# Kernel optimization log

Hardware: AMD Instinct MI355X
Metric: run time of the kernel (lower is better)

The kernel has to match this reference:

```python
import jax, jax.numpy as jnp
import numpy as np

BATCH = 1024
INPUT_DIM = 256
UNITS = 256
GRID_SIZE = 5
SPLINE_ORDER = 3
GRID_LO, GRID_HI = -1.0, 1.0


def _make_grid(dtype):
    # (input_dim, grid_size + 2*spline_order + 1) uniform knot grid, extended
    # by spline_order cells on each side (matches DenseKAN.build)
    bound = GRID_HI - GRID_LO
    g = jnp.linspace(GRID_LO - SPLINE_ORDER * bound / GRID_SIZE,
                     GRID_HI + SPLINE_ORDER * bound / GRID_SIZE,
                     GRID_SIZE + 2 * SPLINE_ORDER + 1, dtype=dtype)
    return jnp.broadcast_to(g[None, :], (INPUT_DIM, g.shape[0]))


def _spline_bases(x, grid):
    # x: (B, in), grid: (in, G+2k+1) -> bases: (B, in, G+k)  (Cox-de Boor)
    xe = x[:, :, None]
    bases = ((xe >= grid[:, :-1]) & (xe < grid[:, 1:])).astype(x.dtype)
    for k in range(1, SPLINE_ORDER + 1):
        left = (xe - grid[:, :-(k + 1)]) / (grid[:, k:-1] - grid[:, :-(k + 1)])
        right = (grid[:, k + 1:] - xe) / (grid[:, k + 1:] - grid[:, 1:-k])
        bases = left * bases[:, :, :-1] + right * bases[:, :, 1:]
    return bases


def setup_inputs() -> dict:
    key = jax.random.key(0)
    k1, k2, k3 = jax.random.split(key, 3)
    x = jax.random.uniform(k1, (BATCH, INPUT_DIM), dtype=jnp.float32,
                           minval=-1.0, maxval=1.0)
    # RandomNormal(stddev=0.1) init for spline_kernel
    spline_kernel = 0.1 * jax.random.normal(
        k2, (INPUT_DIM, GRID_SIZE + SPLINE_ORDER, UNITS), dtype=jnp.float32)
    # GlorotUniform init for scale_factor
    limit = float(np.sqrt(6.0 / (INPUT_DIM + UNITS)))
    scale_factor = jax.random.uniform(k3, (INPUT_DIM, UNITS), dtype=jnp.float32,
                                      minval=-limit, maxval=limit)
    bias = jnp.zeros((UNITS,), dtype=jnp.float32)
    return {"x": x, "spline_kernel": spline_kernel,
            "scale_factor": scale_factor, "bias": bias}


def reference(x, spline_kernel, scale_factor, bias):
    grid = _make_grid(x.dtype)
    bases = _spline_bases(x, grid)                       # (B, in, G+k)
    spline_out = jnp.einsum('bik,iko->bio', bases, spline_kernel)  # (B, in, units)
    spline_out = spline_out + jax.nn.silu(x)[:, :, None]
    spline_out = spline_out * scale_factor[None, :, :]
    out = jnp.sum(spline_out, axis=-2) + bias            # (B, units)
    return out
```

## Files before the change

kernel.cpp:

```cpp
#include <hip/hip_runtime.h>
#include <hip/hip_bf16.h>

#define BATCH   1024
#define IN_DIM  256
#define UNITS   256

using short8 = __attribute__((ext_vector_type(8))) short;
using f32x4  = __attribute__((ext_vector_type(4))) float;

#define A_ELEMS (64 * 72 * 512)
#define W_ELEMS (16 * 72 * 512)

__device__ __forceinline__ unsigned short f2bf(float v) {
    __hip_bfloat16 h = __float2bfloat16(v);
    return *reinterpret_cast<unsigned short*>(&h);
}

__global__ __launch_bounds__(256) void prep_all(const float* __restrict__ X,
                                                const float* __restrict__ SK,
                                                const float* __restrict__ SF,
                                                unsigned short* __restrict__ Ap,
                                                unsigned short* __restrict__ Wp) {
    const int t = threadIdx.x;
    if (blockIdx.x < 256) {
        __shared__ unsigned short tile[18 * 512];
        const int mt = blockIdx.x >> 2;
        const int q  = blockIdx.x & 3;
        #pragma unroll
        for (int rr = 0; rr < 4; ++rr) {
            const int p  = t + 256 * rr;
            const int b  = p >> 6;
            const int il = p & 63;
            const int i  = q * 64 + il;
            const float x = X[(mt * 16 + b) * IN_DIM + i];
            const float u = (x + 2.2f) * 2.5f;
            int j = (int)floorf(u);
            j = j < 3 ? 3 : (j > 7 ? 7 : j);
            const float gj = -2.2f + 0.4f * (float)j;
            const float tt = (x - gj) * 2.5f;
            const float t2 = tt * tt, t3 = t2 * tt;
            const float k6 = 1.f / 6.f;
            const float b0 = (1.f - 3.f * tt + 3.f * t2 - t3) * k6;
            const float b1 = (3.f * t3 - 6.f * t2 + 4.f) * k6;
            const float b2 = (-3.f * t3 + 3.f * t2 + 3.f * tt + 1.f) * k6;
            const float b3 = t3 * k6;
            const float sil = x / (1.f + __expf(-x));
            const int base = j - 3;
            const int kk0  = il * 9;
            #pragma unroll
            for (int kf = 0; kf < 9; ++kf) {
                float v;
                if (kf == 8) v = sil;
                else v = (kf == base)     ? b0
                       : (kf == base + 1) ? b1
                       : (kf == base + 2) ? b2
                       : (kf == base + 3) ? b3 : 0.f;
                const int kkl  = kk0 + kf;
                const int sl   = kkl >> 5;
                const int kpos = kkl & 31;
                tile[sl * 512 + ((b | ((kpos >> 3) << 4)) << 3) + (kpos & 7)] = f2bf(v);
            }
        }
        __syncthreads();
        const unsigned int* src = (const unsigned int*)tile;
        unsigned int* dst = (unsigned int*)Ap + (mt * 72 + 18 * q) * 256;
        #pragma unroll
        for (int k = 0; k < 18; ++k) dst[t + 256 * k] = src[t + 256 * k];
    } else {
        const int slot = (blockIdx.x - 256) * 256 + t;
        const int lane = slot & 63;
        const int s    = (slot >> 6) % 72;
        const int nt   = slot / (72 * 64);
        const int o    = nt * 16 + (lane & 15);
        const int kb   = (lane >> 4) << 3;
        unsigned short r[8];
        #pragma unroll
        for (int e = 0; e < 8; ++e) {
            const int kk = s * 32 + kb + e;
            const int i  = kk / 9;
            const int kf = kk - i * 9;
            const float sfv = SF[i * UNITS + o];
            const float v = (kf < 8) ? SK[(i * 8 + kf) * UNITS + o] * sfv : sfv;
            r[e] = f2bf(v);
        }
        unsigned int pack[4];
        #pragma unroll
        for (int e = 0; e < 4; ++e)
            pack[e] = (unsigned int)r[2 * e] | ((unsigned int)r[2 * e + 1] << 16);
        reinterpret_cast<uint4*>(Wp)[slot] = make_uint4(pack[0], pack[1], pack[2], pack[3]);
    }
}

__global__ __launch_bounds__(512) void kan_gemm(const unsigned short* __restrict__ Ap,
                                                const unsigned short* __restrict__ Wp,
                                                const float* __restrict__ BIAS,
                                                float* __restrict__ OUT) {
    __shared__ float red[8 * 1024];
    const int tid  = threadIdx.x;
    const int w    = tid >> 6;
    const int lane = tid & 63;
    const int m = blockIdx.x & 31;
    const int n = blockIdx.x >> 5;
    const short8* A8 = (const short8*)Ap;
    const short8* W8 = (const short8*)Wp;
    const int mt0 = 2 * m, nt0 = 2 * n;
    const int s0  = 9 * w;

    const short8* pa0 = A8 + (size_t)(mt0 * 72 + s0) * 64 + lane;
    const short8* pa1 = pa0 + 72 * 64;
    const short8* pb0 = W8 + (size_t)(nt0 * 72 + s0) * 64 + lane;
    const short8* pb1 = pb0 + 72 * 64;

    f32x4 acc00 = {0.f, 0.f, 0.f, 0.f}, acc01 = {0.f, 0.f, 0.f, 0.f};
    f32x4 acc10 = {0.f, 0.f, 0.f, 0.f}, acc11 = {0.f, 0.f, 0.f, 0.f};

    short8 a0 = pa0[0], a1 = pa1[0], b0 = pb0[0], b1 = pb1[0];
    #pragma unroll
    for (int it = 0; it < 9; ++it) {
        acc00 = __builtin_amdgcn_mfma_f32_16x16x32_bf16(a0, b0, acc00, 0, 0, 0);
        acc01 = __builtin_amdgcn_mfma_f32_16x16x32_bf16(a0, b1, acc01, 0, 0, 0);
        acc10 = __builtin_amdgcn_mfma_f32_16x16x32_bf16(a1, b0, acc10, 0, 0, 0);
        acc11 = __builtin_amdgcn_mfma_f32_16x16x32_bf16(a1, b1, acc11, 0, 0, 0);
        if (it < 8) {
            a0 = pa0[64 * (it + 1)];
            a1 = pa1[64 * (it + 1)];
            b0 = pb0[64 * (it + 1)];
            b1 = pb1[64 * (it + 1)];
        }
    }

    f32x4* redv = (f32x4*)red;
    redv[(w * 4 + 0) * 64 + lane] = acc00;
    redv[(w * 4 + 1) * 64 + lane] = acc01;
    redv[(w * 4 + 2) * 64 + lane] = acc10;
    redv[(w * 4 + 3) * 64 + lane] = acc11;
    __syncthreads();

    #pragma unroll
    for (int half = 0; half < 2; ++half) {
        const int flat = half * 512 + tid;
        float sum = 0.f;
        #pragma unroll
        for (int w2 = 0; w2 < 8; ++w2) sum += red[w2 * 1024 + flat];
        const int f  = flat >> 8;
        const int l  = (flat >> 2) & 63;
        const int rr = flat & 3;
        const int row = m * 32 + (f >> 1) * 16 + ((l >> 4) << 2) + rr;
        const int col = n * 32 + (f & 1) * 16 + (l & 15);
        OUT[row * UNITS + col] = sum + BIAS[col];
    }
}

__global__ __launch_bounds__(256) void kan_fused(
    const float* __restrict__ X, const float* __restrict__ SK,
    const float* __restrict__ SF, const float* __restrict__ BIAS,
    float* __restrict__ OUT) {
    __shared__ float feat[128][12];
    const int tid  = threadIdx.x;
    const int brow = blockIdx.x * 4;
    const int o    = tid;
    float acc[4] = {0.f, 0.f, 0.f, 0.f};
    for (int c = 0; c < 8; ++c) {
        if (tid < 128) {
            const int ii = tid >> 2;
            const int r  = tid & 3;
            const int i  = c * 32 + ii;
            const float x = X[(size_t)(brow + r) * IN_DIM + i];
            float u = (x + 2.2f) * 2.5f;
            int j = (int)floorf(u);
            j = j < 3 ? 3 : (j > 7 ? 7 : j);
            const float gj = -2.2f + 0.4f * (float)j;
            const float t  = (x - gj) * 2.5f;
            const float t2 = t * t, t3 = t2 * t;
            const float k6 = 1.f / 6.f;
            float* fp = feat[ii * 4 + r];
            #pragma unroll
            for (int k = 0; k < 12; ++k) fp[k] = 0.f;
            const int base = j - 3;
            fp[base + 0] = (1.f - 3.f*t + 3.f*t2 - t3) * k6;
            fp[base + 1] = (3.f*t3 - 6.f*t2 + 4.f) * k6;
            fp[base + 2] = (-3.f*t3 + 3.f*t2 + 3.f*t + 1.f) * k6;
            fp[base + 3] = t3 * k6;
            fp[8] = x / (1.f + __expf(-x));
        }
        __syncthreads();
        #pragma unroll 4
        for (int ii = 0; ii < 32; ++ii) {
            const int i = c * 32 + ii;
            const float* skp = SK + (size_t)i * 8 * UNITS + o;
            const float s0 = skp[0*UNITS], s1 = skp[1*UNITS], s2 = skp[2*UNITS], s3 = skp[3*UNITS];
            const float s4 = skp[4*UNITS], s5 = skp[5*UNITS], s6 = skp[6*UNITS], s7 = skp[7*UNITS];
            const float sfv = SF[(size_t)i * UNITS + o];
            #pragma unroll
            for (int r = 0; r < 4; ++r) {
                const float* fp = feat[ii * 4 + r];
                const float4 fa = *(const float4*)(fp);
                const float4 fb = *(const float4*)(fp + 4);
                float ts = fp[8];
                ts = fmaf(fa.x, s0, ts); ts = fmaf(fa.y, s1, ts);
                ts = fmaf(fa.z, s2, ts); ts = fmaf(fa.w, s3, ts);
                ts = fmaf(fb.x, s4, ts); ts = fmaf(fb.y, s5, ts);
                ts = fmaf(fb.z, s6, ts); ts = fmaf(fb.w, s7, ts);
                acc[r] = fmaf(sfv, ts, acc[r]);
            }
        }
        __syncthreads();
    }
    const float bo = BIAS[o];
    #pragma unroll
    for (int r = 0; r < 4; ++r)
        OUT[(size_t)(brow + r) * UNITS + o] = acc[r] + bo;
}

extern "C" void kernel_launch(void* const* d_in, const int* in_sizes, int n_in,
                              void* d_out, int out_size, void* d_ws, size_t ws_size,
                              hipStream_t stream) {
    const float* X  = (const float*)d_in[0];
    const float* SK = (const float*)d_in[1];
    const float* SF = (const float*)d_in[2];
    const float* B  = (const float*)d_in[3];
    float* OUT = (float*)d_out;

    const size_t need = ((size_t)A_ELEMS + (size_t)W_ELEMS) * 2;
    if (d_ws != nullptr && ws_size >= need) {
        unsigned short* Ap = (unsigned short*)d_ws;
        unsigned short* Wp = Ap + A_ELEMS;
        prep_all<<<dim3(544), dim3(256), 0, stream>>>(X, SK, SF, Ap, Wp);
        kan_gemm<<<dim3(256), dim3(512), 0, stream>>>(Ap, Wp, B, OUT);
    } else {
        kan_fused<<<dim3(BATCH / 4), dim3(256), 0, stream>>>(X, SK, SF, B, OUT);
    }
}
```

Measured before the change: 17.08 us.

## Fuse prep and GEMM kernels into one cooperative launch with grid sync

Merges the operand-packing kernel and the MFMA GEMM into a single cooperative kernel of 256 blocks. The first half of each block builds spline bases into shared memory while the second half packs the scaled weights, then a grid-wide barrier separates packing from the GEMM. This removes one kernel launch and the gap between kernels, at the cost of a grid sync and a different work split for the prep phase. If the cooperative launch fails, it falls back to the original two kernels.

```diff
diff --git a/kernel.cpp b/kernel.cpp
--- a/kernel.cpp
+++ b/kernel.cpp
@@ -1,5 +1,8 @@
 #include <hip/hip_runtime.h>
 #include <hip/hip_bf16.h>
+#include <hip/hip_cooperative_groups.h>
+
+namespace cg = cooperative_groups;
 
 #define BATCH   1024
 #define IN_DIM  256
@@ -14,6 +17,149 @@
 __device__ __forceinline__ unsigned short f2bf(float v) {
     __hip_bfloat16 h = __float2bfloat16(v);
     return *reinterpret_cast<unsigned short*>(&h);
+}
+
+__global__ __launch_bounds__(512, 1) void kan_one(
+    const float* __restrict__ X, const float* __restrict__ SK,
+    const float* __restrict__ SF, const float* __restrict__ BIAS,
+    unsigned short* __restrict__ Ap, unsigned short* __restrict__ Wp,
+    float* __restrict__ OUT)
+{
+    __shared__ __align__(16) unsigned char smem[32768];
+    const int tid = threadIdx.x;
+    const int bid = blockIdx.x;
+
+    unsigned short* tile = (unsigned short*)smem;
+    if (tid < 256) {
+        const int mt = bid >> 2;
+        const int q  = bid & 3;
+        #pragma unroll
+        for (int rr = 0; rr < 4; ++rr) {
+            const int p  = tid + 256 * rr;
+            const int b  = p >> 6;
+            const int il = p & 63;
+            const int i  = q * 64 + il;
+            const float x = X[(mt * 16 + b) * IN_DIM + i];
+            const float u = (x + 2.2f) * 2.5f;
+            int j = (int)floorf(u);
+            j = j < 3 ? 3 : (j > 7 ? 7 : j);
+            const float gj = -2.2f + 0.4f * (float)j;
+            const float tt = (x - gj) * 2.5f;
+            const float t2 = tt * tt, t3 = t2 * tt;
+            const float k6 = 1.f / 6.f;
+            const float b0 = (1.f - 3.f * tt + 3.f * t2 - t3) * k6;
+            const float b1 = (3.f * t3 - 6.f * t2 + 4.f) * k6;
+            const float b2 = (-3.f * t3 + 3.f * t2 + 3.f * tt + 1.f) * k6;
+            const float b3 = t3 * k6;
+            const float sil = x / (1.f + __expf(-x));
+            const int base = j - 3;
+            const int kk0  = il * 9;
+            #pragma unroll
+            for (int kf = 0; kf < 9; ++kf) {
+                float v;
+                if (kf == 8) v = sil;
+                else v = (kf == base)     ? b0
+                       : (kf == base + 1) ? b1
+                       : (kf == base + 2) ? b2
+                       : (kf == base + 3) ? b3 : 0.f;
+                const int kkl  = kk0 + kf;
+                const int sl   = kkl >> 5;
+                const int kpos = kkl & 31;
+                tile[sl * 512 + ((b | ((kpos >> 3) << 4)) << 3) + (kpos & 7)] = f2bf(v);
+            }
+        }
+    } else {
+        const int base_idx = bid * 256 + (tid - 256);
+        #pragma unroll
+        for (int rep = 0; rep < 2; ++rep) {
+            const int slot = base_idx + rep * 65536;
+            if (slot < 73728) {
+                const int lane = slot & 63;
+                const int s    = (slot >> 6) % 72;
+                const int nt   = slot / (72 * 64);
+                const int o    = nt * 16 + (lane & 15);
+                const int kb   = (lane >> 4) << 3;
+                unsigned short r[8];
+                #pragma unroll
+                for (int e = 0; e < 8; ++e) {
+                    const int kk = s * 32 + kb + e;
+                    const int i  = kk / 9;
+                    const int kf = kk - i * 9;
+                    const float sfv = SF[i * UNITS + o];
+                    const float v = (kf < 8) ? SK[(i * 8 + kf) * UNITS + o] * sfv : sfv;
+                    r[e] = f2bf(v);
+                }
+                unsigned int pk[4];
+                #pragma unroll
+                for (int e = 0; e < 4; ++e)
+                    pk[e] = (unsigned int)r[2 * e] | ((unsigned int)r[2 * e + 1] << 16);
+                reinterpret_cast<uint4*>(Wp)[slot] = make_uint4(pk[0], pk[1], pk[2], pk[3]);
+            }
+        }
+    }
+    __syncthreads();
+    {
+        const unsigned int* src = (const unsigned int*)tile;
+        unsigned int* dst = (unsigned int*)Ap + ((bid >> 2) * 72 + 18 * (bid & 3)) * 256;
+        #pragma unroll
+        for (int k = 0; k < 9; ++k) dst[tid + 512 * k] = src[tid + 512 * k];
+    }
+
+    cg::this_grid().sync();
+
+    const int w    = tid >> 6;
+    const int lane = tid & 63;
+    const int m = bid & 31;
+    const int n = bid >> 5;
+    const short8* A8 = (const short8*)Ap;
+    const short8* W8 = (const short8*)Wp;
+    const int mt0 = 2 * m, nt0 = 2 * n;
+    const int s0  = 9 * w;
+
+    const short8* pa0 = A8 + (size_t)(mt0 * 72 + s0) * 64 + lane;
+    const short8* pa1 = pa0 + 72 * 64;
+    const short8* pb0 = W8 + (size_t)(nt0 * 72 + s0) * 64 + lane;
+    const short8* pb1 = pb0 + 72 * 64;
+
+    f32x4 acc00 = {0.f, 0.f, 0.f, 0.f}, acc01 = {0.f, 0.f, 0.f, 0.f};
+    f32x4 acc10 = {0.f, 0.f, 0.f, 0.f}, acc11 = {0.f, 0.f, 0.f, 0.f};
+
+    short8 a0 = pa0[0], a1 = pa1[0], b0 = pb0[0], b1 = pb1[0];
+    #pragma unroll
+    for (int it = 0; it < 9; ++it) {
+        acc00 = __builtin_amdgcn_mfma_f32_16x16x32_bf16(a0, b0, acc00, 0, 0, 0);
+        acc01 = __builtin_amdgcn_mfma_f32_16x16x32_bf16(a0, b1, acc01, 0, 0, 0);
+        acc10 = __builtin_amdgcn_mfma_f32_16x16x32_bf16(a1, b0, acc10, 0, 0, 0);
+        acc11 = __builtin_amdgcn_mfma_f32_16x16x32_bf16(a1, b1, acc11, 0, 0, 0);
+        if (it < 8) {
+            a0 = pa0[64 * (it + 1)];
+            a1 = pa1[64 * (it + 1)];
+            b0 = pb0[64 * (it + 1)];
+            b1 = pb1[64 * (it + 1)];
+        }
+    }
+
+    float* red = (float*)smem;
+    f32x4* redv = (f32x4*)red;
+    redv[(w * 4 + 0) * 64 + lane] = acc00;
+    redv[(w * 4 + 1) * 64 + lane] = acc01;
+    redv[(w * 4 + 2) * 64 + lane] = acc10;
+    redv[(w * 4 + 3) * 64 + lane] = acc11;
+    __syncthreads();
+
+    #pragma unroll
+    for (int half = 0; half < 2; ++half) {
+        const int flat = half * 512 + tid;
+        float sum = 0.f;
+        #pragma unroll
+        for (int w2 = 0; w2 < 8; ++w2) sum += red[w2 * 1024 + flat];
+        const int f  = flat >> 8;
+        const int l  = (flat >> 2) & 63;
+        const int rr = flat & 3;
+        const int row = m * 32 + (f >> 1) * 16 + ((l >> 4) << 2) + rr;
+        const int col = n * 32 + (f & 1) * 16 + (l & 15);
+        OUT[row * UNITS + col] = sum + BIAS[col];
+    }
 }
 
 __global__ __launch_bounds__(256) void prep_all(const float* __restrict__ X,
@@ -105,15 +251,12 @@
     const short8* W8 = (const short8*)Wp;
     const int mt0 = 2 * m, nt0 = 2 * n;
     const int s0  = 9 * w;
-
     const short8* pa0 = A8 + (size_t)(mt0 * 72 + s0) * 64 + lane;
     const short8* pa1 = pa0 + 72 * 64;
     const short8* pb0 = W8 + (size_t)(nt0 * 72 + s0) * 64 + lane;
     const short8* pb1 = pb0 + 72 * 64;
-
-    f32x4 acc00 = {0.f, 0.f, 0.f, 0.f}, acc01 = {0.f, 0.f, 0.f, 0.f};
-    f32x4 acc10 = {0.f, 0.f, 0.f, 0.f}, acc11 = {0.f, 0.f, 0.f, 0.f};
-
+    f32x4 acc00 = {0.f,0.f,0.f,0.f}, acc01 = {0.f,0.f,0.f,0.f};
+    f32x4 acc10 = {0.f,0.f,0.f,0.f}, acc11 = {0.f,0.f,0.f,0.f};
     short8 a0 = pa0[0], a1 = pa1[0], b0 = pb0[0], b1 = pb1[0];
     #pragma unroll
     for (int it = 0; it < 9; ++it) {
@@ -128,14 +271,12 @@
             b1 = pb1[64 * (it + 1)];
         }
     }
-
     f32x4* redv = (f32x4*)red;
     redv[(w * 4 + 0) * 64 + lane] = acc00;
     redv[(w * 4 + 1) * 64 + lane] = acc01;
     redv[(w * 4 + 2) * 64 + lane] = acc10;
     redv[(w * 4 + 3) * 64 + lane] = acc11;
     __syncthreads();
-
     #pragma unroll
     for (int half = 0; half < 2; ++half) {
         const int flat = half * 512 + tid;
@@ -225,8 +366,15 @@
     if (d_ws != nullptr && ws_size >= need) {
         unsigned short* Ap = (unsigned short*)d_ws;
         unsigned short* Wp = Ap + A_ELEMS;
-        prep_all<<<dim3(544), dim3(256), 0, stream>>>(X, SK, SF, Ap, Wp);
-        kan_gemm<<<dim3(256), dim3(512), 0, stream>>>(Ap, Wp, B, OUT);
+        void* args[] = { (void*)&X, (void*)&SK, (void*)&SF, (void*)&B,
+                         (void*)&Ap, (void*)&Wp, (void*)&OUT };
+        hipError_t e = hipLaunchCooperativeKernel((const void*)kan_one,
+                                                  dim3(256), dim3(512),
+                                                  args, 0, stream);
+        if (e != hipSuccess) {
+            prep_all<<<dim3(544), dim3(256), 0, stream>>>(X, SK, SF, Ap, Wp);
+            kan_gemm<<<dim3(256), dim3(512), 0, stream>>>(Ap, Wp, B, OUT);
+        }
     } else {
         kan_fused<<<dim3(BATCH / 4), dim3(256), 0, stream>>>(X, SK, SF, B, OUT);
     }
```

Result: slower. 59.93 us (+250.9%).

## Regroup K layout so each input owns an 8-wide bf16 fragment with silu tail

Applied to the files above, without the earlier changes.

Changes the packed K layout from 9 interleaved entries per input (8 bases + silu) to 8 spline-basis slots per input, with four inputs per 32-wide K slice, and puts all silu terms in 8 trailing slices. Each thread now writes one 16-byte fragment directly to global memory, built with a shift of the four nonzero cubic bases. This removes the LDS staging, scattered 2-byte stores and integer divides of the old prep kernel. The weight prep is split the same way, scaled spline weights in the first 64 slices and scale factors in the tail. The GEMM kernel is unchanged apart from whitespace, and the prep grid grows to 1440 blocks.

```diff
diff --git a/kernel.cpp b/kernel.cpp
--- a/kernel.cpp
+++ b/kernel.cpp
@@ -7,6 +7,7 @@
 
 using short8 = __attribute__((ext_vector_type(8))) short;
 using f32x4  = __attribute__((ext_vector_type(4))) float;
+using u32x4  = __attribute__((ext_vector_type(4))) unsigned int;
 
 #define A_ELEMS (64 * 72 * 512)
 #define W_ELEMS (16 * 72 * 512)
@@ -16,78 +17,105 @@
     return *reinterpret_cast<unsigned short*>(&h);
 }
 
-__global__ __launch_bounds__(256) void prep_all(const float* __restrict__ X,
-                                                const float* __restrict__ SK,
-                                                const float* __restrict__ SF,
-                                                unsigned short* __restrict__ Ap,
-                                                unsigned short* __restrict__ Wp) {
-    const int t = threadIdx.x;
-    if (blockIdx.x < 256) {
-        __shared__ unsigned short tile[18 * 512];
-        const int mt = blockIdx.x >> 2;
-        const int q  = blockIdx.x & 3;
+__device__ __forceinline__ short8 bases_frag(float x) {
+    const float u = fmaf(x, 2.5f, 5.5f);
+    float fj = floorf(u);
+    fj = fj < 3.f ? 3.f : (fj > 7.f ? 7.f : fj);
+    const float t  = u - fj;
+    const float s1 = 1.f - t;
+    const float t2 = t * t;
+    const float t3 = t2 * t;
+    const float b0 = s1 * s1 * s1 * (1.f / 6.f);
+    const float b1 = fmaf(0.5f, t3, fmaf(-1.f, t2, 2.f / 3.f));
+    const float b3 = t3 * (1.f / 6.f);
+    const float b2 = 1.f - b0 - b1 - b3;
+    const unsigned int p01 = (unsigned int)f2bf(b0) | ((unsigned int)f2bf(b1) << 16);
+    const unsigned int p23 = (unsigned int)f2bf(b2) | ((unsigned int)f2bf(b3) << 16);
+    const unsigned long long A = (unsigned long long)p01 | ((unsigned long long)p23 << 32);
+    const int sh = ((int)fj - 3) << 4;
+    const unsigned long long lo = (sh < 64) ? (A << (sh & 63)) : 0ULL;
+    const unsigned long long hi = (sh == 0) ? 0ULL
+                                : ((sh >= 64) ? A : (A >> ((64 - sh) & 63)));
+    u32x4 r;
+    r.x = (unsigned int)lo;  r.y = (unsigned int)(lo >> 32);
+    r.z = (unsigned int)hi;  r.w = (unsigned int)(hi >> 32);
+    return __builtin_bit_cast(short8, r);
+}
+
+__device__ __forceinline__ float silu_f(float x) {
+    return x / (1.f + __expf(-x));
+}
+
+__global__ __launch_bounds__(256) void prep_fast(const float* __restrict__ X,
+                                                 const float* __restrict__ SK,
+                                                 const float* __restrict__ SF,
+                                                 unsigned short* __restrict__ Ap,
+                                                 unsigned short* __restrict__ Wp) {
+    const int tid = threadIdx.x;
+    const int bid = blockIdx.x;
+    if (bid < 1024) {
+        const int mt  = bid >> 4;
+        const int ic  = bid & 15;
+        const int row = tid & 15;
+        const int di  = (tid >> 4) & 3;
+        const int ds  = (tid >> 6) & 3;
+        const int S   = ic * 4 + ds;
+        const int i   = S * 4 + di;
+        const float x = X[(mt * 16 + row) * IN_DIM + i];
+        const short8 f = bases_frag(x);
+        ((short8*)Ap)[(mt * 72 + S) * 64 + (row | (di << 4))] = f;
+    } else if (bid < 1152) {
+        const int b2  = bid - 1024;
+        const int mt  = b2 >> 1;
+        const int row = tid & 15;
+        const int q   = (tid >> 4) & 3;
+        const int i32 = (b2 & 1) * 4 + ((tid >> 6) & 3);
+        const int i0  = i32 * 32 + q * 8;
+        const float* xp = X + (mt * 16 + row) * IN_DIM + i0;
+        const float4 va = *(const float4*)(xp);
+        const float4 vb = *(const float4*)(xp + 4);
+        unsigned int pk[4];
+        pk[0] = (unsigned int)f2bf(silu_f(va.x)) | ((unsigned int)f2bf(silu_f(va.y)) << 16);
+        pk[1] = (unsigned int)f2bf(silu_f(va.z)) | ((unsigned int)f2bf(silu_f(va.w)) << 16);
+        pk[2] = (unsigned int)f2bf(silu_f(vb.x)) | ((unsigned int)f2bf(silu_f(vb.y)) << 16);
+        pk[3] = (unsigned int)f2bf(silu_f(vb.z)) | ((unsigned int)f2bf(silu_f(vb.w)) << 16);
+        u32x4 r = {pk[0], pk[1], pk[2], pk[3]};
+        ((short8*)Ap)[(mt * 72 + 64 + i32) * 64 + (row | (q << 4))] =
+            __builtin_bit_cast(short8, r);
+    } else if (bid < 1408) {
+        const int sl   = (bid - 1152) * 256 + tid;
+        const int lane = sl & 63;
+        const int S    = (sl >> 6) & 63;
+        const int nt   = sl >> 12;
+        const int o    = nt * 16 + (lane & 15);
+        const int i    = S * 4 + (lane >> 4);
+        const float sfv = SF[i * UNITS + o];
+        const float* skp = SK + (size_t)i * 8 * UNITS + o;
+        unsigned int pk[4];
         #pragma unroll
-        for (int rr = 0; rr < 4; ++rr) {
-            const int p  = t + 256 * rr;
-            const int b  = p >> 6;
-            const int il = p & 63;
-            const int i  = q * 64 + il;
-            const float x = X[(mt * 16 + b) * IN_DIM + i];
-            const float u = (x + 2.2f) * 2.5f;
-            int j = (int)floorf(u);
-            j = j < 3 ? 3 : (j > 7 ? 7 : j);
-            const float gj = -2.2f + 0.4f * (float)j;
-            const float tt = (x - gj) * 2.5f;
-            const float t2 = tt * tt, t3 = t2 * tt;
-            const float k6 = 1.f / 6.f;
-            const float b0 = (1.f - 3.f * tt + 3.f * t2 - t3) * k6;
-            const float b1 = (3.f * t3 - 6.f * t2 + 4.f) * k6;
-            const float b2 = (-3.f * t3 + 3.f * t2 + 3.f * tt + 1.f) * k6;
-            const float b3 = t3 * k6;
-            const float sil = x / (1.f + __expf(-x));
-            const int base = j - 3;
-            const int kk0  = il * 9;
-            #pragma unroll
-            for (int kf = 0; kf < 9; ++kf) {
-                float v;
-                if (kf == 8) v = sil;
-                else v = (kf == base)     ? b0
-                       : (kf == base + 1) ? b1
-                       : (kf == base + 2) ? b2
-                       : (kf == base + 3) ? b3 : 0.f;
-                const int kkl  = kk0 + kf;
-                const int sl   = kkl >> 5;
-                const int kpos = kkl & 31;
-                tile[sl * 512 + ((b | ((kpos >> 3) << 4)) << 3) + (kpos & 7)] = f2bf(v);
-            }
-        }
-        __syncthreads();
-        const unsigned int* src = (const unsigned int*)tile;
-        unsigned int* dst = (unsigned int*)Ap + (mt * 72 + 18 * q) * 256;
+        for (int e2 = 0; e2 < 4; ++e2) {
+            const float v0 = skp[(2 * e2    ) * UNITS] * sfv;
+            const float v1 = skp[(2 * e2 + 1) * UNITS] * sfv;
+            pk[e2] = (unsigned int)f2bf(v0) | ((unsigned int)f2bf(v1) << 16);
+        }
+        u32x4 r = {pk[0], pk[1], pk[2], pk[3]};
+        ((short8*)Wp)[(nt * 72 + S) * 64 + lane] = __builtin_bit_cast(short8, r);
+    } else {
+        const int sl   = (bid - 1408) * 256 + tid;
+        const int lane = sl & 63;
+        const int i32  = (sl >> 6) & 7;
+        const int nt   = sl >> 9;
+        const int o    = nt * 16 + (lane & 15);
+        const int i0   = i32 * 32 + (lane >> 4) * 8;
+        unsigned int pk[4];
         #pragma unroll
-        for (int k = 0; k < 18; ++k) dst[t + 256 * k] = src[t + 256 * k];
-    } else {
-        const int slot = (blockIdx.x - 256) * 256 + t;
-        const int lane = slot & 63;
-        const int s    = (slot >> 6) % 72;
-        const int nt   = slot / (72 * 64);
-        const int o    = nt * 16 + (lane & 15);
-        const int kb   = (lane >> 4) << 3;
-        unsigned short r[8];
-        #pragma unroll
-        for (int e = 0; e < 8; ++e) {
-            const int kk = s * 32 + kb + e;
-            const int i  = kk / 9;
-            const int kf = kk - i * 9;
-            const float sfv = SF[i * UNITS + o];
-            const float v = (kf < 8) ? SK[(i * 8 + kf) * UNITS + o] * sfv : sfv;
-            r[e] = f2bf(v);
-        }
-        unsigned int pack[4];
-        #pragma unroll
-        for (int e = 0; e < 4; ++e)
-            pack[e] = (unsigned int)r[2 * e] | ((unsigned int)r[2 * e + 1] << 16);
-        reinterpret_cast<uint4*>(Wp)[slot] = make_uint4(pack[0], pack[1], pack[2], pack[3]);
+        for (int e2 = 0; e2 < 4; ++e2) {
+            const float v0 = SF[(i0 + 2 * e2    ) * UNITS + o];
+            const float v1 = SF[(i0 + 2 * e2 + 1) * UNITS + o];
+            pk[e2] = (unsigned int)f2bf(v0) | ((unsigned int)f2bf(v1) << 16);
+        }
+        u32x4 r = {pk[0], pk[1], pk[2], pk[3]};
+        ((short8*)Wp)[(nt * 72 + 64 + i32) * 64 + lane] = __builtin_bit_cast(short8, r);
     }
 }
 
@@ -105,15 +133,12 @@
     const short8* W8 = (const short8*)Wp;
     const int mt0 = 2 * m, nt0 = 2 * n;
     const int s0  = 9 * w;
-
     const short8* pa0 = A8 + (size_t)(mt0 * 72 + s0) * 64 + lane;
     const short8* pa1 = pa0 + 72 * 64;
     const short8* pb0 = W8 + (size_t)(nt0 * 72 + s0) * 64 + lane;
     const short8* pb1 = pb0 + 72 * 64;
-
-    f32x4 acc00 = {0.f, 0.f, 0.f, 0.f}, acc01 = {0.f, 0.f, 0.f, 0.f};
-    f32x4 acc10 = {0.f, 0.f, 0.f, 0.f}, acc11 = {0.f, 0.f, 0.f, 0.f};
-
+    f32x4 acc00 = {0.f,0.f,0.f,0.f}, acc01 = {0.f,0.f,0.f,0.f};
+    f32x4 acc10 = {0.f,0.f,0.f,0.f}, acc11 = {0.f,0.f,0.f,0.f};
     short8 a0 = pa0[0], a1 = pa1[0], b0 = pb0[0], b1 = pb1[0];
     #pragma unroll
     for (int it = 0; it < 9; ++it) {
@@ -128,14 +153,12 @@
             b1 = pb1[64 * (it + 1)];
         }
     }
-
     f32x4* redv = (f32x4*)red;
     redv[(w * 4 + 0) * 64 + lane] = acc00;
     redv[(w * 4 + 1) * 64 + lane] = acc01;
     redv[(w * 4 + 2) * 64 + lane] = acc10;
     redv[(w * 4 + 3) * 64 + lane] = acc11;
     __syncthreads();
-
     #pragma unroll
     for (int half = 0; half < 2; ++half) {
         const int flat = half * 512 + tid;
@@ -225,7 +248,7 @@
     if (d_ws != nullptr && ws_size >= need) {
         unsigned short* Ap = (unsigned short*)d_ws;
         unsigned short* Wp = Ap + A_ELEMS;
-        prep_all<<<dim3(544), dim3(256), 0, stream>>>(X, SK, SF, Ap, Wp);
+        prep_fast<<<dim3(1440), dim3(256), 0, stream>>>(X, SK, SF, Ap, Wp);
         kan_gemm<<<dim3(256), dim3(512), 0, stream>>>(Ap, Wp, B, OUT);
     } else {
         kan_fused<<<dim3(BATCH / 4), dim3(256), 0, stream>>>(X, SK, SF, B, OUT);
```

New measurement: 16.26 us. 1.05x faster.
